# Kernel tuning notes

Hardware: AMD Instinct MI355X
Metric: run time of the kernel (lower is better)

Reference implementation:

```python
import jax, jax.numpy as jnp
import numpy as np

L = 2        # num GRU layers
H = 1024     # hidden_size
V = 50257    # output_size (vocab)


def setup_inputs() -> dict:
    key = jax.random.key(0)
    ks = jax.random.split(key, 10)
    s = 1.0 / np.sqrt(H)
    return {
        "input_tok": jax.random.randint(ks[0], (1,), 0, V, dtype=jnp.int64),
        "hidden": jax.random.normal(ks[1], (L, 1, H), dtype=jnp.float32),
        "emb": jax.random.normal(ks[2], (V, H), dtype=jnp.float32),
        "W_ih": jax.random.uniform(ks[3], (L, 3 * H, H), jnp.float32, -s, s),
        "W_hh": jax.random.uniform(ks[4], (L, 3 * H, H), jnp.float32, -s, s),
        "b_ih": jax.random.uniform(ks[5], (L, 3 * H), jnp.float32, -s, s),
        "b_hh": jax.random.uniform(ks[6], (L, 3 * H), jnp.float32, -s, s),
        "W_out": jax.random.uniform(ks[7], (V, H), jnp.float32, -s, s),
        "b_out": jax.random.uniform(ks[8], (V,), jnp.float32, -s, s),
    }


def _gru_step(x, hidden, W_ih, W_hh, b_ih, b_hh):
    # x: [1, H] single-timestep input; hidden: [L, 1, H]
    # PyTorch GRU gate order: r, z, n
    new_h = []
    for l in range(L):
        h = hidden[l]                                   # [1, H]
        gi = x @ W_ih[l].T + b_ih[l]                    # [1, 3H]
        gh = h @ W_hh[l].T + b_hh[l]                    # [1, 3H]
        gi_r, gi_z, gi_n = gi[:, :H], gi[:, H:2 * H], gi[:, 2 * H:]
        gh_r, gh_z, gh_n = gh[:, :H], gh[:, H:2 * H], gh[:, 2 * H:]
        r = jax.nn.sigmoid(gi_r + gh_r)
        z = jax.nn.sigmoid(gi_z + gh_z)
        n = jnp.tanh(gi_n + r * gh_n)
        h_new = (1.0 - z) * n + z * h                   # [1, H]
        new_h.append(h_new)
        x = h_new                                       # feed next layer (eval: no dropout)
    return x, jnp.stack(new_h, axis=0)                  # [1,H], [L,1,H]


def reference(input_tok, hidden, emb, W_ih, W_hh, b_ih, b_hh, W_out, b_out):
    # embedding lookup + view(1,1,-1) -> relu
    x = jax.nn.relu(emb[input_tok[0]]).reshape(1, H)     # [1, H] (seq dim of 1 folded)
    out, hidden_new = _gru_step(x, hidden, W_ih, W_hh, b_ih, b_hh)
    logits = out @ W_out.T + b_out                       # [1, V]
    logprobs = jax.nn.log_softmax(logits, axis=1)        # LogSoftmax(dim=1)
    return logprobs, hidden_new
```

## Files before the change

kernel.cpp:

```cpp
#include <hip/hip_runtime.h>
#include <cstdint>
#include <math.h>

#define H 1024
#define V 50257

__device__ __forceinline__ unsigned fenc(float f) {
    unsigned b = __float_as_uint(f);
    return (b & 0x80000000u) ? ~b : (b | 0x80000000u);
}
__device__ __forceinline__ float fdec(unsigned k) {
    unsigned b = (k & 0x80000000u) ? (k ^ 0x80000000u) : ~k;
    return __uint_as_float(b);
}

__device__ __forceinline__ float dot4(float4 a, float4 b) {
    return a.x * b.x + a.y * b.y + a.z * b.z + a.w * b.w;
}

__global__ __launch_bounds__(256) void gru_layer(
    const float* __restrict__ emb, const int* __restrict__ tok, int use_emb,
    const float* __restrict__ xvec,
    const float* __restrict__ hprev,
    const float* __restrict__ Wih, const float* __restrict__ Whh,
    const float* __restrict__ bih, const float* __restrict__ bhh,
    float* __restrict__ hnew_ws, float* __restrict__ hnew_out,
    unsigned* __restrict__ maxkey, float* __restrict__ sumacc, int do_init)
{
    const int i = blockIdx.x;
    const int t = threadIdx.x;
    if (do_init && i == 0 && t == 0) { *maxkey = 0u; *sumacc = 0.0f; }

    const float* xb = use_emb ? (emb + (size_t)tok[0] * (size_t)H) : xvec;
    float4 xv = *(const float4*)(xb + 4 * t);
    if (use_emb) {
        xv.x = fmaxf(xv.x, 0.f); xv.y = fmaxf(xv.y, 0.f);
        xv.z = fmaxf(xv.z, 0.f); xv.w = fmaxf(xv.w, 0.f);
    }

    float s[6];
    {
        const float* r0 = Wih + (size_t)i * H;
        const float* r1 = Wih + (size_t)(H + i) * H;
        const float* r2 = Wih + (size_t)(2 * H + i) * H;
        const float* r3 = Whh + (size_t)i * H;
        const float* r4 = Whh + (size_t)(H + i) * H;
        const float* r5 = Whh + (size_t)(2 * H + i) * H;
        s[0] = dot4(*(const float4*)(r0 + 4 * t), xv);
        s[1] = dot4(*(const float4*)(r1 + 4 * t), xv);
        s[2] = dot4(*(const float4*)(r2 + 4 * t), xv);
        float4 hv = *(const float4*)(hprev + 4 * t);
        s[3] = dot4(*(const float4*)(r3 + 4 * t), hv);
        s[4] = dot4(*(const float4*)(r4 + 4 * t), hv);
        s[5] = dot4(*(const float4*)(r5 + 4 * t), hv);
    }

    #pragma unroll
    for (int m = 1; m < 64; m <<= 1) {
        #pragma unroll
        for (int k = 0; k < 6; ++k) s[k] += __shfl_xor(s[k], m);
    }
    __shared__ float red[4][6];
    const int wv = t >> 6, ln = t & 63;
    if (ln == 0) {
        #pragma unroll
        for (int k = 0; k < 6; ++k) red[wv][k] = s[k];
    }
    __syncthreads();
    if (t == 0) {
        float g[6];
        #pragma unroll
        for (int k = 0; k < 6; ++k)
            g[k] = red[0][k] + red[1][k] + red[2][k] + red[3][k];
        float gir = g[0] + bih[i], giz = g[1] + bih[H + i], gin = g[2] + bih[2 * H + i];
        float ghr = g[3] + bhh[i], ghz = g[4] + bhh[H + i], ghn = g[5] + bhh[2 * H + i];
        float r = 1.f / (1.f + expf(-(gir + ghr)));
        float z = 1.f / (1.f + expf(-(giz + ghz)));
        float n = tanhf(gin + r * ghn);
        float hp = hprev[i];
        float hn = (1.f - z) * n + z * hp;
        hnew_ws[i] = hn;
        hnew_out[i] = hn;
    }
}

__global__ __launch_bounds__(256) void proj_kernel(
    const float* __restrict__ h, const float* __restrict__ Wout,
    const float* __restrict__ bout, float* __restrict__ logits,
    unsigned* __restrict__ maxkey)
{
    const int t = threadIdx.x;
    const int wv = t >> 6, ln = t & 63;
    const int gw = blockIdx.x * 4 + wv;
    const int nw = gridDim.x * 4;

    float4 hr[4];
    #pragma unroll
    for (int j = 0; j < 4; ++j) hr[j] = *(const float4*)(h + 4 * (ln + 64 * j));

    float wmax = -INFINITY;
    for (int v = gw; v < V; v += nw) {
        const float* wrow = Wout + (size_t)v * H;
        float s = 0.f;
        #pragma unroll
        for (int j = 0; j < 4; ++j)
            s += dot4(*(const float4*)(wrow + 4 * (ln + 64 * j)), hr[j]);
        #pragma unroll
        for (int m = 1; m < 64; m <<= 1) s += __shfl_xor(s, m);
        s += bout[v];
        if (ln == 0) logits[v] = s;
        wmax = fmaxf(wmax, s);
    }
    __shared__ float smax[4];
    if (ln == 0) smax[wv] = wmax;
    __syncthreads();
    if (t == 0) {
        float m = fmaxf(fmaxf(smax[0], smax[1]), fmaxf(smax[2], smax[3]));
        atomicMax(maxkey, fenc(m));
    }
}

__global__ __launch_bounds__(256) void sumexp_kernel(
    const float* __restrict__ logits, const unsigned* __restrict__ maxkey,
    float* __restrict__ sumacc)
{
    const float m = fdec(*maxkey);
    float loc = 0.f;
    for (int v = blockIdx.x * 256 + threadIdx.x; v < V; v += gridDim.x * 256)
        loc += expf(logits[v] - m);
    #pragma unroll
    for (int s = 1; s < 64; s <<= 1) loc += __shfl_xor(loc, s);
    __shared__ float sl[4];
    if ((threadIdx.x & 63) == 0) sl[threadIdx.x >> 6] = loc;
    __syncthreads();
    if (threadIdx.x == 0) atomicAdd(sumacc, sl[0] + sl[1] + sl[2] + sl[3]);
}

__global__ __launch_bounds__(256) void finalize_kernel(
    float* __restrict__ logits, const unsigned* __restrict__ maxkey,
    const float* __restrict__ sumacc)
{
    const float m = fdec(*maxkey);
    const float lz = logf(*sumacc);
    for (int v = blockIdx.x * 256 + threadIdx.x; v < V; v += gridDim.x * 256)
        logits[v] = logits[v] - m - lz;
}

extern "C" void kernel_launch(void* const* d_in, const int* in_sizes, int n_in,
                              void* d_out, int out_size, void* d_ws, size_t ws_size,
                              hipStream_t stream) {
    const int*   tok    = (const int*)d_in[0];
    const float* hidden = (const float*)d_in[1];
    const float* emb    = (const float*)d_in[2];
    const float* Wih    = (const float*)d_in[3];
    const float* Whh    = (const float*)d_in[4];
    const float* bih    = (const float*)d_in[5];
    const float* bhh    = (const float*)d_in[6];
    const float* Wout   = (const float*)d_in[7];
    const float* bout   = (const float*)d_in[8];

    float* out = (float*)d_out;
    float* ws  = (float*)d_ws;
    unsigned* maxkey = (unsigned*)ws;
    float* sumacc = ws + 1;
    float* h0 = ws + 8;
    float* h1 = ws + 8 + H;

    gru_layer<<<H, 256, 0, stream>>>(emb, tok, 1, nullptr, hidden,
                                     Wih, Whh, bih, bhh,
                                     h0, out + V, maxkey, sumacc, 1);
    gru_layer<<<H, 256, 0, stream>>>(nullptr, nullptr, 0, h0, hidden + H,
                                     Wih + 3 * H * H, Whh + 3 * H * H,
                                     bih + 3 * H, bhh + 3 * H,
                                     h1, out + V + H, maxkey, sumacc, 0);
    proj_kernel<<<1024, 256, 0, stream>>>(h1, Wout, bout, out, maxkey);
    sumexp_kernel<<<128, 256, 0, stream>>>(out, maxkey, sumacc);
    finalize_kernel<<<128, 256, 0, stream>>>(out, maxkey, sumacc);
}
```

Before: 411.6 us.

## Fuse online softmax stats into projection and merge sumexp into finalize

The projection kernel now keeps a running max and rescaled sum of exponentials per wave, using the online-softmax recurrence. Each block writes its partial max and sum to workspace instead of doing an atomic max. Finalize merges the 2048 partials in every block and subtracts the log-normaliser, so the separate sumexp pass over the logits and one launch go away. The projection grid also grows from 1024 to 2048 blocks, and each row now costs two extra expf calls.

```diff
diff --git a/kernel.cpp b/kernel.cpp
--- a/kernel.cpp
+++ b/kernel.cpp
@@ -4,15 +4,7 @@
 
 #define H 1024
 #define V 50257
-
-__device__ __forceinline__ unsigned fenc(float f) {
-    unsigned b = __float_as_uint(f);
-    return (b & 0x80000000u) ? ~b : (b | 0x80000000u);
-}
-__device__ __forceinline__ float fdec(unsigned k) {
-    unsigned b = (k & 0x80000000u) ? (k ^ 0x80000000u) : ~k;
-    return __uint_as_float(b);
-}
+#define PBLK 2048
 
 __device__ __forceinline__ float dot4(float4 a, float4 b) {
     return a.x * b.x + a.y * b.y + a.z * b.z + a.w * b.w;
@@ -24,12 +16,10 @@
     const float* __restrict__ hprev,
     const float* __restrict__ Wih, const float* __restrict__ Whh,
     const float* __restrict__ bih, const float* __restrict__ bhh,
-    float* __restrict__ hnew_ws, float* __restrict__ hnew_out,
-    unsigned* __restrict__ maxkey, float* __restrict__ sumacc, int do_init)
+    float* __restrict__ hnew_ws, float* __restrict__ hnew_out)
 {
     const int i = blockIdx.x;
     const int t = threadIdx.x;
-    if (do_init && i == 0 && t == 0) { *maxkey = 0u; *sumacc = 0.0f; }
 
     const float* xb = use_emb ? (emb + (size_t)tok[0] * (size_t)H) : xvec;
     float4 xv = *(const float4*)(xb + 4 * t);
@@ -87,18 +77,18 @@
 __global__ __launch_bounds__(256) void proj_kernel(
     const float* __restrict__ h, const float* __restrict__ Wout,
     const float* __restrict__ bout, float* __restrict__ logits,
-    unsigned* __restrict__ maxkey)
+    float* __restrict__ pmax, float* __restrict__ psum)
 {
     const int t = threadIdx.x;
     const int wv = t >> 6, ln = t & 63;
     const int gw = blockIdx.x * 4 + wv;
-    const int nw = gridDim.x * 4;
+    const int nw = PBLK * 4;
 
     float4 hr[4];
     #pragma unroll
     for (int j = 0; j < 4; ++j) hr[j] = *(const float4*)(h + 4 * (ln + 64 * j));
 
-    float wmax = -INFINITY;
+    float wmax = -INFINITY, wsum = 0.f;
     for (int v = gw; v < V; v += nw) {
         const float* wrow = Wout + (size_t)v * H;
         float s = 0.f;
@@ -109,41 +99,56 @@
         for (int m = 1; m < 64; m <<= 1) s += __shfl_xor(s, m);
         s += bout[v];
         if (ln == 0) logits[v] = s;
-        wmax = fmaxf(wmax, s);
+        float nm = fmaxf(wmax, s);
+        wsum = wsum * expf(wmax - nm) + expf(s - nm);
+        wmax = nm;
     }
-    __shared__ float smax[4];
-    if (ln == 0) smax[wv] = wmax;
+    __shared__ float smax[4], ssum[4];
+    if (ln == 0) { smax[wv] = wmax; ssum[wv] = wsum; }
     __syncthreads();
     if (t == 0) {
         float m = fmaxf(fmaxf(smax[0], smax[1]), fmaxf(smax[2], smax[3]));
-        atomicMax(maxkey, fenc(m));
+        float su = 0.f;
+        #pragma unroll
+        for (int w = 0; w < 4; ++w) su += ssum[w] * expf(smax[w] - m);
+        pmax[blockIdx.x] = m;
+        psum[blockIdx.x] = su;
     }
 }
 
-__global__ __launch_bounds__(256) void sumexp_kernel(
-    const float* __restrict__ logits, const unsigned* __restrict__ maxkey,
-    float* __restrict__ sumacc)
+__global__ __launch_bounds__(256) void finalize_kernel(
+    float* __restrict__ logits,
+    const float* __restrict__ pmax, const float* __restrict__ psum)
 {
-    const float m = fdec(*maxkey);
-    float loc = 0.f;
-    for (int v = blockIdx.x * 256 + threadIdx.x; v < V; v += gridDim.x * 256)
-        loc += expf(logits[v] - m);
+    const int t = threadIdx.x;
+    float m = -INFINITY, su = 0.f;
+    for (int i = t; i < PBLK; i += 256) {
+        float om = pmax[i], os = psum[i];
+        float nm = fmaxf(m, om);
+        su = su * expf(m - nm) + os * expf(om - nm);
+        m = nm;
+    }
     #pragma unroll
-    for (int s = 1; s < 64; s <<= 1) loc += __shfl_xor(loc, s);
-    __shared__ float sl[4];
-    if ((threadIdx.x & 63) == 0) sl[threadIdx.x >> 6] = loc;
+    for (int k = 1; k < 64; k <<= 1) {
+        float om = __shfl_xor(m, k), os = __shfl_xor(su, k);
+        float nm = fmaxf(m, om);
+        su = su * expf(m - nm) + os * expf(om - nm);
+        m = nm;
+    }
+    __shared__ float smax[4], ssum[4], slz;
+    if ((t & 63) == 0) { smax[t >> 6] = m; ssum[t >> 6] = su; }
     __syncthreads();
-    if (threadIdx.x == 0) atomicAdd(sumacc, sl[0] + sl[1] + sl[2] + sl[3]);
-}
-
-__global__ __launch_bounds__(256) void finalize_kernel(
-    float* __restrict__ logits, const unsigned* __restrict__ maxkey,
-    const float* __restrict__ sumacc)
-{
-    const float m = fdec(*maxkey);
-    const float lz = logf(*sumacc);
-    for (int v = blockIdx.x * 256 + threadIdx.x; v < V; v += gridDim.x * 256)
-        logits[v] = logits[v] - m - lz;
+    if (t == 0) {
+        float mm = fmaxf(fmaxf(smax[0], smax[1]), fmaxf(smax[2], smax[3]));
+        float ss = 0.f;
+        #pragma unroll
+        for (int w = 0; w < 4; ++w) ss += ssum[w] * expf(smax[w] - mm);
+        slz = mm + logf(ss);
+    }
+    __syncthreads();
+    const float lz = slz;
+    for (int v = blockIdx.x * 256 + t; v < V; v += gridDim.x * 256)
+        logits[v] = logits[v] - lz;
 }
 
 extern "C" void kernel_launch(void* const* d_in, const int* in_sizes, int n_in,
@@ -161,19 +166,16 @@
 
     float* out = (float*)d_out;
     float* ws  = (float*)d_ws;
-    unsigned* maxkey = (unsigned*)ws;
-    float* sumacc = ws + 1;
-    float* h0 = ws + 8;
-    float* h1 = ws + 8 + H;
+    float* pmax = ws;
+    float* psum = ws + PBLK;
+    float* h0 = ws + 2 * PBLK;
+    float* h1 = ws + 2 * PBLK + H;
 
     gru_layer<<<H, 256, 0, stream>>>(emb, tok, 1, nullptr, hidden,
-                                     Wih, Whh, bih, bhh,
-                                     h0, out + V, maxkey, sumacc, 1);
+                                     Wih, Whh, bih, bhh, h0, out + V);
     gru_layer<<<H, 256, 0, stream>>>(nullptr, nullptr, 0, h0, hidden + H,
                                      Wih + 3 * H * H, Whh + 3 * H * H,
-                                     bih + 3 * H, bhh + 3 * H,
-                                     h1, out + V + H, maxkey, sumacc, 0);
-    proj_kernel<<<1024, 256, 0, stream>>>(h1, Wout, bout, out, maxkey);
-    sumexp_kernel<<<128, 256, 0, stream>>>(out, maxkey, sumacc);
-    finalize_kernel<<<128, 256, 0, stream>>>(out, maxkey, sumacc);
+                                     bih + 3 * H, bhh + 3 * H, h1, out + V + H);
+    proj_kernel<<<PBLK, 256, 0, stream>>>(h1, Wout, bout, out, pmax, psum);
+    finalize_kernel<<<256, 256, 0, stream>>>(out, pmax, psum);
 }
```

New measurement: 411.5 us. About the same (-0.0%).
